# Performance work log

Hardware: AMD Instinct MI355X
Metric: run time of the kernel (lower is better)

## Reference

```python
import jax, jax.numpy as jnp
import numpy as np

NFEAT = 256
N_HEAD = 8
CTXS = (31, 61)
HPS = N_HEAD // len(CTXS)  # heads per scale = 4


def _scale_out(query, value, W1, W2, W3, ctx):
    # query, value: [B, T, F]; W1: [F, F]; W2: [F, HPS*ctx]; W3: [F, F]
    B, T, F = query.shape
    q = jnp.maximum(query @ W1, 0.0)                      # relu(w1(query))
    attn = jax.nn.softmax((q @ W2).reshape(B, T, HPS, ctx), axis=-1)  # [B,T,HPS,ctx]
    half = (ctx - 1) // 2
    v = jnp.pad(value @ W3, ((0, 0), (half, half), (0, 0)))  # [B, T+ctx-1, F]
    idx = jnp.arange(T)[:, None] + jnp.arange(ctx)[None, :]  # [T, ctx] window indices
    vw = v[:, idx]                                          # [B, T, ctx, F]
    vw = vw.reshape(B, T, ctx, HPS, F // HPS)               # per-head dim = F/HPS
    out = jnp.einsum('bthc,btchd->bthd', attn, vw)          # [B,T,HPS,F/HPS]
    return out.reshape(B, T, F)


def setup_inputs() -> dict:
    key = jax.random.key(0)
    ks = jax.random.split(key, 12)
    B, T, F = 2, 4096, NFEAT
    s = 0.02
    return {
        'query': jax.random.normal(ks[0], (B, T, F), jnp.float32),
        'key':   jax.random.normal(ks[1], (B, T, F), jnp.float32),
        'value': jax.random.normal(ks[2], (B, T, F), jnp.float32),
        'w1_0': jax.random.normal(ks[3], (F, F), jnp.float32) * s,
        'w1_1': jax.random.normal(ks[4], (F, F), jnp.float32) * s,
        'w2_0': jax.random.normal(ks[5], (F, HPS * CTXS[0]), jnp.float32) * s,
        'w2_1': jax.random.normal(ks[6], (F, HPS * CTXS[1]), jnp.float32) * s,
        'w3_0': jax.random.normal(ks[7], (F, F), jnp.float32) * s,
        'w3_1': jax.random.normal(ks[8], (F, F), jnp.float32) * s,
        'scale_w': jnp.ones((2,), jnp.float32) / 2.0,
        'w_out': jax.random.normal(ks[9], (F, F), jnp.float32) * s,
    }


def reference(query, key, value, w1_0, w1_1, w2_0, w2_1, w3_0, w3_1, scale_w, w_out):
    sw = jax.nn.softmax(scale_w)
    out = sw[0] * _scale_out(query, value, w1_0, w2_0, w3_0, CTXS[0])
    out = out + sw[1] * _scale_out(query, value, w1_1, w2_1, w3_1, CTXS[1])
    return out @ w_out
```

## Files before the change

kernel.cpp:

```cpp
#include <hip/hip_runtime.h>
#include <hip/hip_bf16.h>
#include <type_traits>

static constexpr int T    = 4096;
static constexpr int F    = 256;
static constexpr int M    = 2 * T;
static constexpr int HPS  = 4;
static constexpr int CTX0 = 31, CTX1 = 61;
static constexpr int LGN  = 384;

typedef short bf16x8 __attribute__((ext_vector_type(8)));
typedef float f32x4  __attribute__((ext_vector_type(4)));

__device__ __forceinline__ ushort f2bf(float f) {
    union { float f; uint u; } v; v.f = f;
    uint u = v.u;
    return (ushort)((u + 0x7fffu + ((u >> 16) & 1u)) >> 16);
}
__device__ __forceinline__ float asf(uint u) {
    union { uint u; float f; } v; v.u = u; return v.f;
}
__device__ __forceinline__ float bf2f(ushort u) { return asf(((uint)u) << 16); }

static constexpr size_t W1T_OFF  = 0;
static constexpr size_t W2B_OFF  = W1T_OFF + (size_t)512 * 256;
static constexpr size_t W3T_OFF  = W2B_OFF + (size_t)384 * 512;
static constexpr size_t WOT_OFF  = W3T_OFF + (size_t)512 * 256;
static constexpr size_t WT_ELEMS = WOT_OFF + (size_t)256 * 256;

struct WArgs {
    const float* w1_0; const float* w1_1;
    const float* w2_0; const float* w2_1;
    const float* w3_0; const float* w3_1;
    const float* wo;
    ushort* wt;
};

__global__ __launch_bounds__(256) void wprep_kernel(WArgs a) {
    __shared__ float tb[64][72];
    const int tid = threadIdx.x;
    const int blk = blockIdx.x;

    const float* src = nullptr;
    ushort* dst; int dstLD, k0, nbase; bool isw2 = false;

    if (blk < 64) {
        int sec = blk >> 4;
        int tt = blk & 15, kt = tt >> 2, nt = tt & 3;
        k0 = kt * 64;
        src = (sec == 0) ? a.w1_0 : (sec == 1) ? a.w1_1 : (sec == 2) ? a.w3_0 : a.w3_1;
        dst = a.wt + ((sec < 2) ? W1T_OFF : W3T_OFF);
        nbase = (sec & 1) * 256 + nt * 64;
        dstLD = 256;
    } else if (blk < 80) {
        int tt = blk - 64, kt = tt >> 2, nt = tt & 3;
        k0 = kt * 64; src = a.wo; dst = a.wt + WOT_OFF; nbase = nt * 64; dstLD = 256;
    } else {
        int tt = blk - 80;
        int nt = tt >> 3, kt = tt & 7;
        k0 = kt * 64; nbase = nt * 64; dst = a.wt + W2B_OFF; dstLD = 512; isw2 = true;
    }

    {
        int kk = tid >> 2;
        int c4 = (tid & 3) * 16;
        if (!isw2) {
            int ncol0 = (blk < 64) ? (nbase & 255) : nbase;
            const float* sp = src + (size_t)(k0 + kk) * 256 + ncol0 + c4;
#pragma unroll
            for (int ii = 0; ii < 4; ii++) {
                float4 v = *reinterpret_cast<const float4*>(sp + ii * 4);
                tb[kk][c4 + ii * 4 + 0] = v.x; tb[kk][c4 + ii * 4 + 1] = v.y;
                tb[kk][c4 + ii * 4 + 2] = v.z; tb[kk][c4 + ii * 4 + 3] = v.w;
            }
        } else {
            int k = k0 + kk;
#pragma unroll 4
            for (int ii = 0; ii < 16; ii++) {
                int n = nbase + c4 + ii;
                float v = 0.f;
                if (n < 124) { if (k < 256) v = a.w2_0[(size_t)k * 124 + n]; }
                else if (n < 368) { if (k >= 256) v = a.w2_1[(size_t)(k - 256) * 244 + (n - 124)]; }
                tb[kk][c4 + ii] = v;
            }
        }
    }
    __syncthreads();

#pragma unroll
    for (int it = 0; it < 2; it++) {
        int slot = it * 256 + tid;
        int n = slot >> 3, ch = slot & 7;
        ushort o[8];
#pragma unroll
        for (int j = 0; j < 8; j++) o[j] = f2bf(tb[ch * 8 + j][n]);
        *reinterpret_cast<bf16x8*>(dst + (size_t)(nbase + n) * dstLD + k0 + ch * 8) =
            *reinterpret_cast<bf16x8*>(o);
    }
}

struct GemmArgs {
    const void* A0; const void* A1; const void* A2;
    const ushort* B0; const ushort* B1;
    void* C0; void* C1;
    int lda, N, ncb, relu0, relu1;
};

template <int KTOT, int AMODE, int NPAIR, typename OutT>
__global__ __launch_bounds__(256, 2) void gemm128_kernel(GemmArgs a) {
    __shared__ ushort Al[2][128][64];
    __shared__ ushort Bl[2][128][64];

    const int tid = threadIdx.x;
    int lin = blockIdx.x;
    int half = gridDim.x;
    int sel = 0;
    if constexpr (NPAIR == 2) {
        half >>= 1;
        sel = lin >= half;
        lin -= sel * half;
    }
    const int qq  = half >> 3;
    const int swz = (lin & 7) * qq + (lin >> 3);
    const int cb  = swz % a.ncb;
    const int rb  = swz / a.ncb;
    const int m0  = rb * 128;
    const int n0  = cb * 128;

    const void*   Av  = sel ? a.A1 : a.A0;
    const ushort* Bt  = sel ? a.B1 : a.B0;
    OutT*         C   = (OutT*)(sel ? a.C1 : a.C0);
    const bool    relu = sel ? (a.relu1 != 0) : (a.relu0 != 0);
    const int     lda = a.lda, N = a.N;

    const int wave = tid >> 6, lane = tid & 63;
    const int wr = wave >> 1, wc = wave & 1;
    const int l15 = lane & 15, l4 = lane >> 4;
    const int srow = tid >> 3;
    const int sch  = tid & 7;

    float4 pAf[4][2];
    bf16x8 pAb[4];
    bf16x8 pA2[4];
    bf16x8 pB[4];

    auto loadRegs = [&](int s) {
        const int k0 = s * 64;
#pragma unroll
        for (int it = 0; it < 4; it++) {
            int row = it * 32 + srow;
            if constexpr (AMODE == 1) {
                const float* ap = (const float*)Av + (size_t)(m0 + row) * lda + k0 + sch * 8;
                pAf[it][0] = *reinterpret_cast<const float4*>(ap);
                pAf[it][1] = *reinterpret_cast<const float4*>(ap + 4);
            } else {
                pAb[it] = *reinterpret_cast<const bf16x8*>(
                    (const ushort*)Av + (size_t)(m0 + row) * lda + k0 + sch * 8);
                if constexpr (AMODE == 2)
                    pA2[it] = *reinterpret_cast<const bf16x8*>(
                        (const ushort*)a.A2 + (size_t)(m0 + row) * lda + k0 + sch * 8);
            }
            pB[it] = *reinterpret_cast<const bf16x8*>(
                Bt + (size_t)(n0 + row) * KTOT + k0 + sch * 8);
        }
    };
    auto writeLds = [&](int buf) {
#pragma unroll
        for (int it = 0; it < 4; it++) {
            int row = it * 32 + srow;
            int c8  = (sch ^ (row & 7)) * 8;
            bf16x8 av;
            if constexpr (AMODE == 1) {
                ushort o[8] = { f2bf(pAf[it][0].x), f2bf(pAf[it][0].y),
                                f2bf(pAf[it][0].z), f2bf(pAf[it][0].w),
                                f2bf(pAf[it][1].x), f2bf(pAf[it][1].y),
                                f2bf(pAf[it][1].z), f2bf(pAf[it][1].w) };
                av = *reinterpret_cast<bf16x8*>(o);
            } else if constexpr (AMODE == 2) {
                ushort o[8];
#pragma unroll
                for (int j = 0; j < 8; j++)
                    o[j] = f2bf(bf2f((ushort)pAb[it][j]) + bf2f((ushort)pA2[it][j]));
                av = *reinterpret_cast<bf16x8*>(o);
            } else {
                av = pAb[it];
            }
            *reinterpret_cast<bf16x8*>(&Al[buf][row][c8]) = av;
            *reinterpret_cast<bf16x8*>(&Bl[buf][row][c8]) = pB[it];
        }
    };

    f32x4 acc[4][4] = {};

    loadRegs(0);
    writeLds(0);
    constexpr int NST = KTOT / 64;
#pragma unroll
    for (int s = 0; s < NST; s++) {
        if (s + 1 < NST) loadRegs(s + 1);
        __syncthreads();
        if (s + 1 < NST) writeLds((s + 1) & 1);
        const int buf = s & 1;
#pragma unroll
        for (int ks = 0; ks < 2; ks++) {
            bf16x8 af[4], bv[4];
#pragma unroll
            for (int i = 0; i < 4; i++) {
                int row = wr * 64 + i * 16 + l15;
                int ch  = (ks * 4 + l4) ^ (row & 7);
                af[i] = *reinterpret_cast<const bf16x8*>(&Al[buf][row][ch * 8]);
            }
#pragma unroll
            for (int j = 0; j < 4; j++) {
                int row = wc * 64 + j * 16 + l15;
                int ch  = (ks * 4 + l4) ^ (row & 7);
                bv[j] = *reinterpret_cast<const bf16x8*>(&Bl[buf][row][ch * 8]);
            }
#pragma unroll
            for (int i = 0; i < 4; i++)
#pragma unroll
                for (int j = 0; j < 4; j++)
                    acc[i][j] = __builtin_amdgcn_mfma_f32_16x16x32_bf16(af[i], bv[j], acc[i][j], 0, 0, 0);
        }
    }

#pragma unroll
    for (int i = 0; i < 4; i++)
#pragma unroll
        for (int j = 0; j < 4; j++) {
            int col = n0 + wc * 64 + j * 16 + l15;
#pragma unroll
            for (int r = 0; r < 4; r++) {
                int row = m0 + wr * 64 + i * 16 + l4 * 4 + r;
                float v = acc[i][j][r];
                if (relu) v = fmaxf(v, 0.0f);
                if constexpr (std::is_same<OutT, ushort>::value)
                    C[(size_t)row * N + col] = f2bf(v);
                else
                    C[(size_t)row * N + col] = v;
            }
        }
}

__global__ __launch_bounds__(256) void attn_kernel(
    const float*  __restrict__ lg,
    const ushort* __restrict__ v01,
    const float*  __restrict__ scale_w,
    ushort*       __restrict__ p0,
    ushort*       __restrict__ p1)
{
    __shared__ ushort vl[92][256];
    __shared__ float  att[32][HPS * CTX1];

    const int tid  = threadIdx.x;
    const int half = gridDim.x >> 1;
    int lin = blockIdx.x;
    const int sc = lin >= half;
    lin -= sc * half;
    const int qq  = half >> 3;
    const int swz = (lin & 7) * qq + (lin >> 3);
    const int bt0 = swz * 32;
    const int b   = bt0 >> 12;
    const int t0  = bt0 & (T - 1);

    const int CTX  = sc ? CTX1 : CTX0;
    const int HALO = (CTX - 1) >> 1;
    const int VR   = 32 + 2 * HALO;
    const int LGO  = sc ? 124 : 0;
    const int VOFF = sc ? 256 : 0;
    ushort* p = sc ? p1 : p0;

    for (int i = tid; i < VR * 32; i += 256) {
        int row = i >> 5, ch = i & 31;
        int tt = t0 - HALO + row;
        bf16x8 v = {};
        if ((unsigned)tt < (unsigned)T)
            v = *reinterpret_cast<const bf16x8*>(
                v01 + ((size_t)(b * T + tt) * 512 + VOFF + ch * 8));
        *reinterpret_cast<bf16x8*>(&vl[row][ch * 8]) = v;
    }

    float s0 = scale_w[0], s1 = scale_w[1];
    float mxs = fmaxf(s0, s1);
    float e0 = __expf(s0 - mxs), e1 = __expf(s1 - mxs);
    float sw = (sc ? e1 : e0) / (e0 + e1);

    {
        int task = tid >> 1, sub = tid & 1;
        int tok = task >> 2, h = task & 3;
        const float* lp = lg + (size_t)(bt0 + tok) * LGN + LGO + h * CTX;
        float* dst = &att[tok][h * CTX];
        float mx = -1e30f;
        for (int c = sub; c < CTX; c += 2) mx = fmaxf(mx, lp[c]);
        mx = fmaxf(mx, __shfl_xor(mx, 1));
        float s = 0.f;
        for (int c = sub; c < CTX; c += 2) {
            float e = __expf(lp[c] - mx);
            dst[c] = e; s += e;
        }
        s += __shfl_xor(s, 1);
        float scl = sw / s;
        for (int c = sub; c < CTX; c += 2) dst[c] *= scl;
    }
    __syncthreads();

    const int w  = tid >> 5;
    const int f0 = (tid & 31) * 8;
    const int h  = f0 >> 6;

#pragma unroll 1
    for (int tk = 0; tk < 4; tk++) {
        int tok = tk * 8 + w;
        const float* aw = &att[tok][h * CTX];
        float acc[8] = {};
#pragma unroll 4
        for (int c = 0; c < CTX; c++) {
            float wv = aw[c];
            uint4 u = *reinterpret_cast<const uint4*>(&vl[tok + c][f0]);
            acc[0] += wv * asf(u.x << 16); acc[1] += wv * asf(u.x & 0xffff0000u);
            acc[2] += wv * asf(u.y << 16); acc[3] += wv * asf(u.y & 0xffff0000u);
            acc[4] += wv * asf(u.z << 16); acc[5] += wv * asf(u.z & 0xffff0000u);
            acc[6] += wv * asf(u.w << 16); acc[7] += wv * asf(u.w & 0xffff0000u);
        }
        ushort o[8];
#pragma unroll
        for (int j = 0; j < 8; j++) o[j] = f2bf(acc[j]);
        *reinterpret_cast<bf16x8*>(p + (size_t)(bt0 + tok) * F + f0) =
            *reinterpret_cast<bf16x8*>(o);
    }
}

extern "C" void kernel_launch(void* const* d_in, const int* in_sizes, int n_in,
                              void* d_out, int out_size, void* d_ws, size_t ws_size,
                              hipStream_t stream)
{
    const float* Q    = (const float*)d_in[0];
    const float* V    = (const float*)d_in[2];
    const float* W1_0 = (const float*)d_in[3];
    const float* W1_1 = (const float*)d_in[4];
    const float* W2_0 = (const float*)d_in[5];
    const float* W2_1 = (const float*)d_in[6];
    const float* W3_0 = (const float*)d_in[7];
    const float* W3_1 = (const float*)d_in[8];
    const float* SW   = (const float*)d_in[9];
    const float* WO   = (const float*)d_in[10];

    char* pws = (char*)d_ws;
    auto carve = [&](size_t bytes) { char* r = pws; pws += (bytes + 255) & ~255ull; return r; };
    ushort* wt  = (ushort*)carve(WT_ELEMS * 2);
    ushort* q01 = (ushort*)carve((size_t)M * 512 * 2);
    float*  lg  = (float*) carve((size_t)M * LGN * 4);
    ushort* v01 = (ushort*)carve((size_t)M * 512 * 2);
    ushort* p0  = (ushort*)carve((size_t)M * F * 2);
    ushort* p1  = (ushort*)carve((size_t)M * F * 2);
    (void)ws_size;

    const ushort* w1t   = wt + W1T_OFF;
    const ushort* w2blk = wt + W2B_OFF;
    const ushort* w3t   = wt + W3T_OFF;
    const ushort* wot   = wt + WOT_OFF;

    wprep_kernel<<<128, 256, 0, stream>>>(
        WArgs{ W1_0, W1_1, W2_0, W2_1, W3_0, W3_1, WO, wt });

    {
        GemmArgs ga{};
        ga.A0 = Q;  ga.A1 = V;  ga.A2 = nullptr;
        ga.B0 = w1t; ga.B1 = w3t;
        ga.C0 = q01; ga.C1 = v01;
        ga.lda = 256; ga.N = 512; ga.ncb = 4; ga.relu0 = 1; ga.relu1 = 0;
        gemm128_kernel<256, 1, 2, ushort><<<512, 256, 0, stream>>>(ga);
    }
    {
        GemmArgs ga{};
        ga.A0 = q01; ga.B0 = w2blk; ga.C0 = lg;
        ga.lda = 512; ga.N = LGN; ga.ncb = 3; ga.relu0 = 0;
        gemm128_kernel<512, 0, 1, float><<<192, 256, 0, stream>>>(ga);
    }
    attn_kernel<<<512, 256, 0, stream>>>(lg, v01, SW, p0, p1);
    {
        GemmArgs ga{};
        ga.A0 = p0; ga.A2 = p1; ga.B0 = wot; ga.C0 = d_out;
        ga.lda = 256; ga.N = 256; ga.ncb = 2; ga.relu0 = 0;
        gemm128_kernel<256, 2, 1, float><<<128, 256, 0, stream>>>(ga);
    }
}
```

Baseline: 140.5 us.

## Fuse logits GEMM, softmax, windowed attention and output projection into one kernel

Replaces the logits GEMM, the attention kernel and the output-projection GEMM with a single fused kernel. Each block handles 32 tokens: it computes the logits with MFMA from q in LDS, runs the softmax in LDS, accumulates both scales' windowed sums in registers, then multiplies by w_out and writes the result. This removes the fp32 logits and the p0/p1 round trips through global memory along with two launches. In exchange the grid shrinks to 256 blocks with heavy LDS use, so occupancy drops, and the two scales now run one after the other inside each block.

```diff
diff --git a/kernel.cpp b/kernel.cpp
--- a/kernel.cpp
+++ b/kernel.cpp
@@ -7,7 +7,6 @@
 static constexpr int M    = 2 * T;
 static constexpr int HPS  = 4;
 static constexpr int CTX0 = 31, CTX1 = 61;
-static constexpr int LGN  = 384;
 
 typedef short bf16x8 __attribute__((ext_vector_type(8)));
 typedef float f32x4  __attribute__((ext_vector_type(4)));
@@ -100,26 +99,22 @@
 }
 
 struct GemmArgs {
-    const void* A0; const void* A1; const void* A2;
+    const void* A0; const void* A1;
     const ushort* B0; const ushort* B1;
     void* C0; void* C1;
     int lda, N, ncb, relu0, relu1;
 };
 
-template <int KTOT, int AMODE, int NPAIR, typename OutT>
+template <int KTOT, typename OutT>
 __global__ __launch_bounds__(256, 2) void gemm128_kernel(GemmArgs a) {
     __shared__ ushort Al[2][128][64];
     __shared__ ushort Bl[2][128][64];
 
     const int tid = threadIdx.x;
     int lin = blockIdx.x;
-    int half = gridDim.x;
-    int sel = 0;
-    if constexpr (NPAIR == 2) {
-        half >>= 1;
-        sel = lin >= half;
-        lin -= sel * half;
-    }
+    int half = gridDim.x >> 1;
+    int sel = lin >= half;
+    lin -= sel * half;
     const int qq  = half >> 3;
     const int swz = (lin & 7) * qq + (lin >> 3);
     const int cb  = swz % a.ncb;
@@ -127,7 +122,7 @@
     const int m0  = rb * 128;
     const int n0  = cb * 128;
 
-    const void*   Av  = sel ? a.A1 : a.A0;
+    const float*  Av  = (const float*)(sel ? a.A1 : a.A0);
     const ushort* Bt  = sel ? a.B1 : a.B0;
     OutT*         C   = (OutT*)(sel ? a.C1 : a.C0);
     const bool    relu = sel ? (a.relu1 != 0) : (a.relu0 != 0);
@@ -140,8 +135,6 @@
     const int sch  = tid & 7;
 
     float4 pAf[4][2];
-    bf16x8 pAb[4];
-    bf16x8 pA2[4];
     bf16x8 pB[4];
 
     auto loadRegs = [&](int s) {
@@ -149,17 +142,9 @@
 #pragma unroll
         for (int it = 0; it < 4; it++) {
             int row = it * 32 + srow;
-            if constexpr (AMODE == 1) {
-                const float* ap = (const float*)Av + (size_t)(m0 + row) * lda + k0 + sch * 8;
-                pAf[it][0] = *reinterpret_cast<const float4*>(ap);
-                pAf[it][1] = *reinterpret_cast<const float4*>(ap + 4);
-            } else {
-                pAb[it] = *reinterpret_cast<const bf16x8*>(
-                    (const ushort*)Av + (size_t)(m0 + row) * lda + k0 + sch * 8);
-                if constexpr (AMODE == 2)
-                    pA2[it] = *reinterpret_cast<const bf16x8*>(
-                        (const ushort*)a.A2 + (size_t)(m0 + row) * lda + k0 + sch * 8);
-            }
+            const float* ap = Av + (size_t)(m0 + row) * lda + k0 + sch * 8;
+            pAf[it][0] = *reinterpret_cast<const float4*>(ap);
+            pAf[it][1] = *reinterpret_cast<const float4*>(ap + 4);
             pB[it] = *reinterpret_cast<const bf16x8*>(
                 Bt + (size_t)(n0 + row) * KTOT + k0 + sch * 8);
         }
@@ -169,23 +154,11 @@
         for (int it = 0; it < 4; it++) {
             int row = it * 32 + srow;
             int c8  = (sch ^ (row & 7)) * 8;
-            bf16x8 av;
-            if constexpr (AMODE == 1) {
-                ushort o[8] = { f2bf(pAf[it][0].x), f2bf(pAf[it][0].y),
-                                f2bf(pAf[it][0].z), f2bf(pAf[it][0].w),
-                                f2bf(pAf[it][1].x), f2bf(pAf[it][1].y),
-                                f2bf(pAf[it][1].z), f2bf(pAf[it][1].w) };
-                av = *reinterpret_cast<bf16x8*>(o);
-            } else if constexpr (AMODE == 2) {
-                ushort o[8];
-#pragma unroll
-                for (int j = 0; j < 8; j++)
-                    o[j] = f2bf(bf2f((ushort)pAb[it][j]) + bf2f((ushort)pA2[it][j]));
-                av = *reinterpret_cast<bf16x8*>(o);
-            } else {
-                av = pAb[it];
-            }
-            *reinterpret_cast<bf16x8*>(&Al[buf][row][c8]) = av;
+            ushort o[8] = { f2bf(pAf[it][0].x), f2bf(pAf[it][0].y),
+                            f2bf(pAf[it][0].z), f2bf(pAf[it][0].w),
+                            f2bf(pAf[it][1].x), f2bf(pAf[it][1].y),
+                            f2bf(pAf[it][1].z), f2bf(pAf[it][1].w) };
+            *reinterpret_cast<bf16x8*>(&Al[buf][row][c8]) = *reinterpret_cast<bf16x8*>(o);
             *reinterpret_cast<bf16x8*>(&Bl[buf][row][c8]) = pB[it];
         }
     };
@@ -234,99 +207,164 @@
                 int row = m0 + wr * 64 + i * 16 + l4 * 4 + r;
                 float v = acc[i][j][r];
                 if (relu) v = fmaxf(v, 0.0f);
-                if constexpr (std::is_same<OutT, ushort>::value)
-                    C[(size_t)row * N + col] = f2bf(v);
-                else
-                    C[(size_t)row * N + col] = v;
+                C[(size_t)row * N + col] = f2bf(v);
             }
         }
 }
 
-__global__ __launch_bounds__(256) void attn_kernel(
-    const float*  __restrict__ lg,
+__global__ __launch_bounds__(256) void fused_kernel(
+    const ushort* __restrict__ q01,
     const ushort* __restrict__ v01,
+    const ushort* __restrict__ w2blk,
+    const ushort* __restrict__ wot,
     const float*  __restrict__ scale_w,
-    ushort*       __restrict__ p0,
-    ushort*       __restrict__ p1)
+    float*        __restrict__ out)
 {
+    __shared__ ushort qs[32][512];
+    __shared__ float  lgs[32][372];
     __shared__ ushort vl[92][256];
-    __shared__ float  att[32][HPS * CTX1];
-
-    const int tid  = threadIdx.x;
-    const int half = gridDim.x >> 1;
-    int lin = blockIdx.x;
-    const int sc = lin >= half;
-    lin -= sc * half;
-    const int qq  = half >> 3;
+
+    const int tid = threadIdx.x;
+    const int lin = blockIdx.x;
+    const int qq  = gridDim.x >> 3;
     const int swz = (lin & 7) * qq + (lin >> 3);
     const int bt0 = swz * 32;
     const int b   = bt0 >> 12;
     const int t0  = bt0 & (T - 1);
 
-    const int CTX  = sc ? CTX1 : CTX0;
-    const int HALO = (CTX - 1) >> 1;
-    const int VR   = 32 + 2 * HALO;
-    const int LGO  = sc ? 124 : 0;
-    const int VOFF = sc ? 256 : 0;
-    ushort* p = sc ? p1 : p0;
-
-    for (int i = tid; i < VR * 32; i += 256) {
+    const int wave = tid >> 6, lane = tid & 63;
+    const int l15 = lane & 15, l4 = lane >> 4;
+
+    for (int i = tid; i < 32 * 64; i += 256) {
+        int row = i >> 6, ch = i & 63;
+        bf16x8 v = *reinterpret_cast<const bf16x8*>(q01 + (size_t)(bt0 + row) * 512 + ch * 8);
+        *reinterpret_cast<bf16x8*>(&qs[row][(ch ^ (row & 7)) * 8]) = v;
+    }
+    for (int i = tid; i < 62 * 32; i += 256) {
         int row = i >> 5, ch = i & 31;
-        int tt = t0 - HALO + row;
+        int tt = t0 - 15 + row;
         bf16x8 v = {};
         if ((unsigned)tt < (unsigned)T)
-            v = *reinterpret_cast<const bf16x8*>(
-                v01 + ((size_t)(b * T + tt) * 512 + VOFF + ch * 8));
+            v = *reinterpret_cast<const bf16x8*>(v01 + (size_t)(b * T + tt) * 512 + ch * 8);
         *reinterpret_cast<bf16x8*>(&vl[row][ch * 8]) = v;
     }
+    __syncthreads();
+
+    for (int ct = wave; ct < 23; ct += 4) {
+        f32x4 acc0 = {}, acc1 = {};
+#pragma unroll
+        for (int ks = 0; ks < 16; ks++) {
+            int ch = (ks * 4 + l4) ^ (l15 & 7);
+            bf16x8 a0 = *reinterpret_cast<const bf16x8*>(&qs[l15][ch * 8]);
+            bf16x8 a1 = *reinterpret_cast<const bf16x8*>(&qs[16 + l15][ch * 8]);
+            bf16x8 bv = *reinterpret_cast<const bf16x8*>(
+                w2blk + (size_t)(ct * 16 + l15) * 512 + ks * 32 + l4 * 8);
+            acc0 = __builtin_amdgcn_mfma_f32_16x16x32_bf16(a0, bv, acc0, 0, 0, 0);
+            acc1 = __builtin_amdgcn_mfma_f32_16x16x32_bf16(a1, bv, acc1, 0, 0, 0);
+        }
+#pragma unroll
+        for (int r = 0; r < 4; r++) {
+            lgs[l4 * 4 + r][ct * 16 + l15]      = acc0[r];
+            lgs[16 + l4 * 4 + r][ct * 16 + l15] = acc1[r];
+        }
+    }
+    __syncthreads();
 
     float s0 = scale_w[0], s1 = scale_w[1];
     float mxs = fmaxf(s0, s1);
     float e0 = __expf(s0 - mxs), e1 = __expf(s1 - mxs);
-    float sw = (sc ? e1 : e0) / (e0 + e1);
+    float sw0 = e0 / (e0 + e1), sw1 = e1 / (e0 + e1);
 
     {
-        int task = tid >> 1, sub = tid & 1;
-        int tok = task >> 2, h = task & 3;
-        const float* lp = lg + (size_t)(bt0 + tok) * LGN + LGO + h * CTX;
-        float* dst = &att[tok][h * CTX];
+        int tok = tid >> 3, j = tid & 7;
+        int sc = j >> 2, h = j & 3;
+        int ctx = sc ? CTX1 : CTX0;
+        float sw = sc ? sw1 : sw0;
+        float* lp = &lgs[tok][sc ? 124 + h * CTX1 : h * CTX0];
         float mx = -1e30f;
-        for (int c = sub; c < CTX; c += 2) mx = fmaxf(mx, lp[c]);
-        mx = fmaxf(mx, __shfl_xor(mx, 1));
+        for (int c = 0; c < ctx; c++) mx = fmaxf(mx, lp[c]);
         float s = 0.f;
-        for (int c = sub; c < CTX; c += 2) {
-            float e = __expf(lp[c] - mx);
-            dst[c] = e; s += e;
-        }
-        s += __shfl_xor(s, 1);
+        for (int c = 0; c < ctx; c++) { float e = __expf(lp[c] - mx); lp[c] = e; s += e; }
         float scl = sw / s;
-        for (int c = sub; c < CTX; c += 2) dst[c] *= scl;
-    }
-    __syncthreads();
-
-    const int w  = tid >> 5;
-    const int f0 = (tid & 31) * 8;
-    const int h  = f0 >> 6;
-
-#pragma unroll 1
+        for (int c = 0; c < ctx; c++) lp[c] *= scl;
+    }
+    __syncthreads();
+
+    const int wgr = tid >> 5;
+    const int f0  = (tid & 31) * 8;
+    const int h   = f0 >> 6;
+    float fa[4][8] = {};
+
+#pragma unroll
     for (int tk = 0; tk < 4; tk++) {
-        int tok = tk * 8 + w;
-        const float* aw = &att[tok][h * CTX];
-        float acc[8] = {};
-#pragma unroll 4
-        for (int c = 0; c < CTX; c++) {
+        int tok = tk * 8 + wgr;
+        const float* aw = &lgs[tok][h * CTX0];
+        for (int c = 0; c < CTX0; c++) {
             float wv = aw[c];
             uint4 u = *reinterpret_cast<const uint4*>(&vl[tok + c][f0]);
-            acc[0] += wv * asf(u.x << 16); acc[1] += wv * asf(u.x & 0xffff0000u);
-            acc[2] += wv * asf(u.y << 16); acc[3] += wv * asf(u.y & 0xffff0000u);
-            acc[4] += wv * asf(u.z << 16); acc[5] += wv * asf(u.z & 0xffff0000u);
-            acc[6] += wv * asf(u.w << 16); acc[7] += wv * asf(u.w & 0xffff0000u);
-        }
+            fa[tk][0] += wv * asf(u.x << 16); fa[tk][1] += wv * asf(u.x & 0xffff0000u);
+            fa[tk][2] += wv * asf(u.y << 16); fa[tk][3] += wv * asf(u.y & 0xffff0000u);
+            fa[tk][4] += wv * asf(u.z << 16); fa[tk][5] += wv * asf(u.z & 0xffff0000u);
+            fa[tk][6] += wv * asf(u.w << 16); fa[tk][7] += wv * asf(u.w & 0xffff0000u);
+        }
+    }
+    __syncthreads();
+
+    for (int i = tid; i < 92 * 32; i += 256) {
+        int row = i >> 5, ch = i & 31;
+        int tt = t0 - 30 + row;
+        bf16x8 v = {};
+        if ((unsigned)tt < (unsigned)T)
+            v = *reinterpret_cast<const bf16x8*>(v01 + (size_t)(b * T + tt) * 512 + 256 + ch * 8);
+        *reinterpret_cast<bf16x8*>(&vl[row][ch * 8]) = v;
+    }
+    __syncthreads();
+
+#pragma unroll
+    for (int tk = 0; tk < 4; tk++) {
+        int tok = tk * 8 + wgr;
+        const float* aw = &lgs[tok][124 + h * CTX1];
+        for (int c = 0; c < CTX1; c++) {
+            float wv = aw[c];
+            uint4 u = *reinterpret_cast<const uint4*>(&vl[tok + c][f0]);
+            fa[tk][0] += wv * asf(u.x << 16); fa[tk][1] += wv * asf(u.x & 0xffff0000u);
+            fa[tk][2] += wv * asf(u.y << 16); fa[tk][3] += wv * asf(u.y & 0xffff0000u);
+            fa[tk][4] += wv * asf(u.z << 16); fa[tk][5] += wv * asf(u.z & 0xffff0000u);
+            fa[tk][6] += wv * asf(u.w << 16); fa[tk][7] += wv * asf(u.w & 0xffff0000u);
+        }
+    }
+    __syncthreads();
+
+    ushort* psumb = &qs[0][0];
+#pragma unroll
+    for (int tk = 0; tk < 4; tk++) {
+        int tok = tk * 8 + wgr;
         ushort o[8];
 #pragma unroll
-        for (int j = 0; j < 8; j++) o[j] = f2bf(acc[j]);
-        *reinterpret_cast<bf16x8*>(p + (size_t)(bt0 + tok) * F + f0) =
+        for (int j = 0; j < 8; j++) o[j] = f2bf(fa[tk][j]);
+        int ch = f0 >> 3;
+        *reinterpret_cast<bf16x8*>(psumb + tok * 256 + ((ch ^ (tok & 7)) * 8)) =
             *reinterpret_cast<bf16x8*>(o);
+    }
+    __syncthreads();
+
+    for (int ct = wave; ct < 16; ct += 4) {
+        f32x4 acc0 = {}, acc1 = {};
+#pragma unroll
+        for (int ks = 0; ks < 8; ks++) {
+            int ch = (ks * 4 + l4) ^ (l15 & 7);
+            bf16x8 a0 = *reinterpret_cast<const bf16x8*>(psumb + l15 * 256 + ch * 8);
+            bf16x8 a1 = *reinterpret_cast<const bf16x8*>(psumb + (16 + l15) * 256 + ch * 8);
+            bf16x8 bv = *reinterpret_cast<const bf16x8*>(
+                wot + (size_t)(ct * 16 + l15) * 256 + ks * 32 + l4 * 8);
+            acc0 = __builtin_amdgcn_mfma_f32_16x16x32_bf16(a0, bv, acc0, 0, 0, 0);
+            acc1 = __builtin_amdgcn_mfma_f32_16x16x32_bf16(a1, bv, acc1, 0, 0, 0);
+        }
+#pragma unroll
+        for (int r = 0; r < 4; r++) {
+            out[(size_t)(bt0 + l4 * 4 + r) * 256 + ct * 16 + l15]      = acc0[r];
+            out[(size_t)(bt0 + 16 + l4 * 4 + r) * 256 + ct * 16 + l15] = acc1[r];
+        }
     }
 }
 
@@ -349,10 +387,7 @@
     auto carve = [&](size_t bytes) { char* r = pws; pws += (bytes + 255) & ~255ull; return r; };
     ushort* wt  = (ushort*)carve(WT_ELEMS * 2);
     ushort* q01 = (ushort*)carve((size_t)M * 512 * 2);
-    float*  lg  = (float*) carve((size_t)M * LGN * 4);
     ushort* v01 = (ushort*)carve((size_t)M * 512 * 2);
-    ushort* p0  = (ushort*)carve((size_t)M * F * 2);
-    ushort* p1  = (ushort*)carve((size_t)M * F * 2);
     (void)ws_size;
 
     const ushort* w1t   = wt + W1T_OFF;
@@ -365,23 +400,12 @@
 
     {
         GemmArgs ga{};
-        ga.A0 = Q;  ga.A1 = V;  ga.A2 = nullptr;
+        ga.A0 = Q;  ga.A1 = V;
         ga.B0 = w1t; ga.B1 = w3t;
         ga.C0 = q01; ga.C1 = v01;
         ga.lda = 256; ga.N = 512; ga.ncb = 4; ga.relu0 = 1; ga.relu1 = 0;
-        gemm128_kernel<256, 1, 2, ushort><<<512, 256, 0, stream>>>(ga);
-    }
-    {
-        GemmArgs ga{};
-        ga.A0 = q01; ga.B0 = w2blk; ga.C0 = lg;
-        ga.lda = 512; ga.N = LGN; ga.ncb = 3; ga.relu0 = 0;
-        gemm128_kernel<512, 0, 1, float><<<192, 256, 0, stream>>>(ga);
-    }
-    attn_kernel<<<512, 256, 0, stream>>>(lg, v01, SW, p0, p1);
-    {
-        GemmArgs ga{};
-        ga.A0 = p0; ga.A2 = p1; ga.B0 = wot; ga.C0 = d_out;
-        ga.lda = 256; ga.N = 256; ga.ncb = 2; ga.relu0 = 0;
-        gemm128_kernel<256, 2, 1, float><<<128, 256, 0, stream>>>(ga);
-    }
-}
+        gemm128_kernel<256, ushort><<<512, 256, 0, stream>>>(ga);
+    }
+
+    fused_kernel<<<256, 256, 0, stream>>>(q01, v01, w2blk, wot, SW, (float*)d_out);
+}
```

Measured after the change: 150.0 us. +6.7%, slower.
